# Kernel tuning notes

Measured on AMD Instinct MI355X. Metric: run time of the kernel, lower is better.

## Reference

```python
import jax, jax.numpy as jnp
import numpy as np

H_DIM = 64      # input_dim of edge_aggregation (== h_dim)
HID = 128       # hidden_size of each per-edge-type agg MLP
T = 5           # edge_types for non-nba dataset
B, E, N = 64, 1024, 512


def setup_inputs() -> dict:
    key = jax.random.key(0)
    ks = jax.random.split(key, 8)
    edge_distribution = jax.random.uniform(ks[0], (B, E, T), dtype=jnp.float32)
    H = jax.random.uniform(ks[1], (B, E, N), dtype=jnp.float32)
    ori = jax.random.normal(ks[2], (B, N, H_DIM), dtype=jnp.float32)
    s1 = 1.0 / np.sqrt(H_DIM)
    s2 = 1.0 / np.sqrt(HID)
    # stacked per-edge-type MLP params: Linear(64->128) -> ReLU -> Linear(128->64)
    W1 = jax.random.uniform(ks[3], (T, H_DIM, HID), minval=-s1, maxval=s1, dtype=jnp.float32)
    b1 = jax.random.uniform(ks[4], (T, HID), minval=-s1, maxval=s1, dtype=jnp.float32)
    W2 = jax.random.uniform(ks[5], (T, HID, H_DIM), minval=-s2, maxval=s2, dtype=jnp.float32)
    b2 = jax.random.uniform(ks[6], (T, H_DIM), minval=-s2, maxval=s2, dtype=jnp.float32)
    return {"edge_distribution": edge_distribution, "H": H, "ori": ori,
            "W1": W1, "b1": b1, "W2": W2, "b2": b2}


def reference(edge_distribution, H, ori, W1, b1, W2, b2):
    # incidence gather: hyperedge features [B, E, D]
    edges = jnp.matmul(H, ori)
    # per-edge-type 2-layer MLP, vectorized over the T edge types
    h = jax.nn.relu(jnp.einsum('bed,tdh->bteh', edges, W1) + b1[None, :, None, :])
    per_type = jnp.einsum('bteh,thd->bted', h, W2) + b2[None, :, None, :]
    # mixture-weighted sum over edge types -> [B, E, D]
    edge_feature = jnp.einsum('bet,bted->bed', edge_distribution, per_type)
    # scatter back through H^T and concat with original node features
    node_agg = jnp.einsum('ben,bed->bnd', H, edge_feature)  # H^T @ edge_feature
    node_feature = jnp.concatenate((node_agg, ori), axis=-1)  # [B, N, 2D]
    return node_feature
```

## Files before the change

### kernel.cpp

```cpp
#include <hip/hip_runtime.h>

#define B_   64
#define E_   1024
#define N_   512
#define D_   64
#define HID_ 128
#define T_   5

typedef __bf16 bf16x8 __attribute__((ext_vector_type(8)));
typedef float f32x4 __attribute__((ext_vector_type(4)));

__device__ __forceinline__ unsigned short f2bu(float f) {
    union { float f; unsigned int u; } v; v.f = f;
    unsigned int r = (v.u + 0x7fffu + ((v.u >> 16) & 1u)) >> 16;
    return (unsigned short)r;
}

__device__ __forceinline__ unsigned int pack2(float lo, float hi) {
    union { __bf16 b[2]; unsigned int u; } v;
    v.b[0] = (__bf16)lo; v.b[1] = (__bf16)hi;
    return v.u;
}

__device__ __forceinline__ uint4 cvt8(float4 a, float4 b) {
    union { __bf16 h[8]; uint4 u; } v;
    v.h[0] = (__bf16)a.x; v.h[1] = (__bf16)a.y; v.h[2] = (__bf16)a.z; v.h[3] = (__bf16)a.w;
    v.h[4] = (__bf16)b.x; v.h[5] = (__bf16)b.y; v.h[6] = (__bf16)b.z; v.h[7] = (__bf16)b.w;
    return v.u;
}

#define MFMA16(a, b, c) __builtin_amdgcn_mfma_f32_16x16x32_bf16((a), (b), (c), 0, 0, 0)

__global__ __launch_bounds__(256) void k_prep_w(const float* __restrict__ W1,
                                                const float* __restrict__ W2,
                                                unsigned short* __restrict__ W1T,
                                                unsigned short* __restrict__ W2T) {
    int idx = blockIdx.x * 256 + threadIdx.x;
    if (idx < T_ * HID_ * D_) {
        int t = idx / (HID_ * D_), rem = idx % (HID_ * D_);
        int h = rem / D_, d = rem % D_;
        W1T[idx] = f2bu(W1[(t * D_ + d) * HID_ + h]);
    } else {
        int j = idx - T_ * HID_ * D_;
        int t = j / (D_ * HID_), rem = j % (D_ * HID_);
        int d = rem / HID_, h = rem % HID_;
        W2T[j] = f2bu(W2[(t * HID_ + h) * D_ + d]);
    }
}

__global__ __launch_bounds__(256) void k_ori_prep(const float* __restrict__ ori,
                                                  float* __restrict__ out,
                                                  unsigned short* __restrict__ oriT) {
    int b = blockIdx.y, n0 = blockIdx.x * 64;
    __shared__ float tl[64 * 65];
    int tid = threadIdx.x;
    int dl = tid & 63;
    #pragma unroll 4
    for (int p = 0; p < 16; ++p) {
        int nn = p * 4 + (tid >> 6);
        float v = ori[(size_t)(b * N_ + n0 + nn) * D_ + dl];
        out[(size_t)(b * N_ + n0 + nn) * 128 + 64 + dl] = v;
        tl[dl * 65 + nn] = v;
    }
    __syncthreads();
    #pragma unroll 4
    for (int p = 0; p < 16; ++p) {
        int dd = p * 4 + (tid >> 6);
        oriT[(size_t)(b * D_ + dd) * N_ + n0 + dl] = f2bu(tl[dd * 65 + dl]);
    }
}

__global__ __launch_bounds__(256) void k_gemm_edges(const float* __restrict__ H,
                                                    const unsigned short* __restrict__ oriT,
                                                    unsigned short* __restrict__ edges) {
    int b = blockIdx.y, e0 = blockIdx.x * 128;
    __shared__ __align__(16) unsigned short aA[128 * 72];
    __shared__ __align__(16) unsigned short bB[64 * 72];
    int tid = threadIdx.x, w = tid >> 6, l = tid & 63, q = l >> 4, c = l & 15;
    const f32x4 zero = {0.f, 0.f, 0.f, 0.f};
    f32x4 acc[2][4];
    #pragma unroll
    for (int fm = 0; fm < 2; ++fm)
        #pragma unroll
        for (int fn = 0; fn < 4; ++fn) acc[fm][fn] = zero;

    for (int ks = 0; ks < 8; ++ks) {
        int k0 = ks * 64;
        #pragma unroll
        for (int p = 0; p < 4; ++p) {
            int u = p * 256 + tid, r = u >> 3, sg = u & 7;
            const float* s = &H[((size_t)b * E_ + e0 + r) * N_ + k0 + sg * 8];
            float4 f0 = *(const float4*)&s[0];
            float4 f1 = *(const float4*)&s[4];
            *(uint4*)&aA[r * 72 + sg * 8] = cvt8(f0, f1);
        }
        #pragma unroll
        for (int p = 0; p < 2; ++p) {
            int u = p * 256 + tid, r = u >> 3, sg = u & 7;
            *(uint4*)&bB[r * 72 + sg * 8] =
                *(const uint4*)&oriT[((size_t)b * D_ + r) * N_ + k0 + sg * 8];
        }
        __syncthreads();
        #pragma unroll
        for (int h = 0; h < 2; ++h) {
            bf16x8 a0 = *(const bf16x8*)&aA[(w * 32 + c) * 72 + h * 32 + q * 8];
            bf16x8 a1 = *(const bf16x8*)&aA[(w * 32 + 16 + c) * 72 + h * 32 + q * 8];
            #pragma unroll
            for (int fn = 0; fn < 4; ++fn) {
                bf16x8 bb = *(const bf16x8*)&bB[(fn * 16 + c) * 72 + h * 32 + q * 8];
                acc[0][fn] = MFMA16(a0, bb, acc[0][fn]);
                acc[1][fn] = MFMA16(a1, bb, acc[1][fn]);
            }
        }
        __syncthreads();
    }
    #pragma unroll
    for (int fm = 0; fm < 2; ++fm)
        #pragma unroll
        for (int fn = 0; fn < 4; ++fn)
            #pragma unroll
            for (int i = 0; i < 4; ++i) {
                int e = e0 + w * 32 + fm * 16 + q * 4 + i;
                int d = fn * 16 + c;
                edges[((size_t)b * E_ + e) * D_ + d] = f2bu(acc[fm][fn][i]);
            }
}

__global__ __launch_bounds__(256) void k_mlp(const unsigned short* __restrict__ edges,
                                             const float* __restrict__ ed,
                                             const float* __restrict__ b1,
                                             const float* __restrict__ b2,
                                             const unsigned short* __restrict__ W1T,
                                             const unsigned short* __restrict__ W2T,
                                             unsigned short* __restrict__ efT) {
    int bx = blockIdx.x;
    int b = bx >> 4, e0 = (bx & 15) * 64;
    __shared__ __align__(16) unsigned short a_sh[64 * 72];
    __shared__ __align__(16) unsigned short w_sh[128 * 72];
    __shared__ __align__(16) unsigned short h_sh[64 * 136];
    __shared__ float wd_sh[320];
    __shared__ float b1_sh[640];
    __shared__ float b2_sh[320];
    int tid = threadIdx.x, w = tid >> 6, l = tid & 63, q = l >> 4, c = l & 15;

    #pragma unroll
    for (int p = 0; p < 2; ++p) {
        int u = p * 256 + tid, r = u >> 3, sg = u & 7;
        *(uint4*)&a_sh[r * 72 + sg * 8] =
            *(const uint4*)&edges[((size_t)b * E_ + e0 + r) * D_ + sg * 8];
    }
    for (int u = tid; u < 320; u += 256) wd_sh[u] = ed[((size_t)b * E_ + e0) * T_ + u];
    for (int u = tid; u < 640; u += 256) b1_sh[u] = b1[u];
    for (int u = tid; u < 320; u += 256) b2_sh[u] = b2[u];

    const f32x4 zero = {0.f, 0.f, 0.f, 0.f};
    f32x4 y[4];
    #pragma unroll
    for (int fn = 0; fn < 4; ++fn) y[fn] = zero;

    for (int t = 0; t < T_; ++t) {
        __syncthreads();
        #pragma unroll
        for (int p = 0; p < 4; ++p) {
            int u = p * 256 + tid, hh = u >> 3, sg = u & 7;
            *(uint4*)&w_sh[hh * 72 + sg * 8] =
                *(const uint4*)&W1T[(t * HID_ + hh) * D_ + sg * 8];
        }
        __syncthreads();
        f32x4 hc[8];
        #pragma unroll
        for (int fn = 0; fn < 8; ++fn) hc[fn] = zero;
        #pragma unroll
        for (int ks = 0; ks < 2; ++ks) {
            bf16x8 a = *(const bf16x8*)&a_sh[(w * 16 + c) * 72 + ks * 32 + q * 8];
            #pragma unroll
            for (int fn = 0; fn < 8; ++fn) {
                bf16x8 bb = *(const bf16x8*)&w_sh[(fn * 16 + c) * 72 + ks * 32 + q * 8];
                hc[fn] = MFMA16(a, bb, hc[fn]);
            }
        }
        float wv[4];
        #pragma unroll
        for (int i = 0; i < 4; ++i) wv[i] = wd_sh[(w * 16 + q * 4 + i) * T_ + t];
        #pragma unroll
        for (int fn = 0; fn < 8; ++fn) {
            float b1v = b1_sh[t * HID_ + fn * 16 + c];
            #pragma unroll
            for (int i = 0; i < 4; ++i) {
                float v = hc[fn][i] + b1v;
                v = fmaxf(v, 0.0f) * wv[i];
                h_sh[(w * 16 + q * 4 + i) * 136 + fn * 16 + c] = f2bu(v);
            }
        }
        __syncthreads();
        #pragma unroll
        for (int p = 0; p < 4; ++p) {
            int u = p * 256 + tid, dd = u >> 4, sg = u & 15;
            *(uint4*)&w_sh[dd * 136 + sg * 8] =
                *(const uint4*)&W2T[(t * D_ + dd) * HID_ + sg * 8];
        }
        __syncthreads();
        #pragma unroll
        for (int ks = 0; ks < 4; ++ks) {
            bf16x8 a = *(const bf16x8*)&h_sh[(w * 16 + c) * 136 + ks * 32 + q * 8];
            #pragma unroll
            for (int fn = 0; fn < 4; ++fn) {
                bf16x8 bb = *(const bf16x8*)&w_sh[(fn * 16 + c) * 136 + ks * 32 + q * 8];
                y[fn] = MFMA16(a, bb, y[fn]);
            }
        }
    }
    #pragma unroll
    for (int fn = 0; fn < 4; ++fn) {
        int d = fn * 16 + c;
        ushort4 o;
        #pragma unroll
        for (int i = 0; i < 4; ++i) {
            int r = w * 16 + q * 4 + i;
            float s = y[fn][i];
            #pragma unroll
            for (int t = 0; t < T_; ++t) s += wd_sh[r * T_ + t] * b2_sh[t * D_ + d];
            ((unsigned short*)&o)[i] = f2bu(s);
        }
        *(ushort4*)&efT[((size_t)b * D_ + d) * E_ + e0 + w * 16 + q * 4] = o;
    }
}

__global__ __launch_bounds__(256) void k_gemm_out(const float* __restrict__ H,
                                                  const unsigned short* __restrict__ efT,
                                                  float* __restrict__ out) {
    int b = blockIdx.y, n0 = blockIdx.x * 64;
    __shared__ __align__(16) unsigned short aA[64 * 72];
    __shared__ unsigned int bB32[64 * 33];
    int tid = threadIdx.x, w = tid >> 6, l = tid & 63, q = l >> 4, c = l & 15;
    int r2 = tid >> 3, cg = tid & 7;
    const f32x4 zero = {0.f, 0.f, 0.f, 0.f};
    f32x4 acc[4];
    #pragma unroll
    for (int fm = 0; fm < 4; ++fm) acc[fm] = zero;

    for (int ks = 0; ks < 16; ++ks) {
        int k0 = ks * 64;
        #pragma unroll
        for (int p = 0; p < 2; ++p) {
            int u = p * 256 + tid, r = u >> 3, sg = u & 7;
            *(uint4*)&aA[r * 72 + sg * 8] =
                *(const uint4*)&efT[((size_t)b * D_ + r) * E_ + k0 + sg * 8];
        }
        {
            const float* s0 = &H[((size_t)b * E_ + k0 + 2 * r2) * N_ + n0 + cg * 8];
            const float* s1 = s0 + N_;
            float4 f0 = *(const float4*)&s0[0], f1 = *(const float4*)&s0[4];
            float4 g0 = *(const float4*)&s1[0], g1 = *(const float4*)&s1[4];
            float r0[8] = {f0.x, f0.y, f0.z, f0.w, f1.x, f1.y, f1.z, f1.w};
            float r1[8] = {g0.x, g0.y, g0.z, g0.w, g1.x, g1.y, g1.z, g1.w};
            #pragma unroll
            for (int j = 0; j < 8; ++j)
                bB32[(cg * 8 + j) * 33 + r2] = pack2(r0[j], r1[j]);
        }
        __syncthreads();
        #pragma unroll
        for (int h = 0; h < 2; ++h) {
            union { unsigned int u[4]; bf16x8 v; } bb;
            #pragma unroll
            for (int i = 0; i < 4; ++i)
                bb.u[i] = bB32[(w * 16 + c) * 33 + h * 16 + q * 4 + i];
            #pragma unroll
            for (int fm = 0; fm < 4; ++fm) {
                bf16x8 afr = *(const bf16x8*)&aA[(fm * 16 + c) * 72 + h * 32 + q * 8];
                acc[fm] = MFMA16(afr, bb.v, acc[fm]);
            }
        }
        __syncthreads();
    }
    #pragma unroll
    for (int fm = 0; fm < 4; ++fm) {
        *(f32x4*)&out[((size_t)b * N_ + n0 + w * 16 + c) * 128 + fm * 16 + q * 4] = acc[fm];
    }
}

extern "C" void kernel_launch(void* const* d_in, const int* in_sizes, int n_in,
                              void* d_out, int out_size, void* d_ws, size_t ws_size,
                              hipStream_t stream) {
    const float* ed  = (const float*)d_in[0];
    const float* H   = (const float*)d_in[1];
    const float* ori = (const float*)d_in[2];
    const float* W1  = (const float*)d_in[3];
    const float* b1  = (const float*)d_in[4];
    const float* W2  = (const float*)d_in[5];
    const float* b2  = (const float*)d_in[6];
    float* out = (float*)d_out;

    char* ws = (char*)d_ws;
    unsigned short* oriT  = (unsigned short*)ws; ws += (size_t)B_ * D_ * N_ * 2;
    unsigned short* W1T   = (unsigned short*)ws; ws += (size_t)T_ * HID_ * D_ * 2;
    unsigned short* W2T   = (unsigned short*)ws; ws += (size_t)T_ * D_ * HID_ * 2;
    unsigned short* edges = (unsigned short*)ws; ws += (size_t)B_ * E_ * D_ * 2;
    unsigned short* efT   = (unsigned short*)ws; ws += (size_t)B_ * D_ * E_ * 2;

    hipLaunchKernelGGL(k_prep_w, dim3(320), dim3(256), 0, stream, W1, W2, W1T, W2T);
    hipLaunchKernelGGL(k_ori_prep, dim3(8, 64), dim3(256), 0, stream, ori, out, oriT);
    hipLaunchKernelGGL(k_gemm_edges, dim3(8, 64), dim3(256), 0, stream, H, oriT, edges);
    hipLaunchKernelGGL(k_mlp, dim3(1024), dim3(256), 0, stream, edges, ed, b1, b2, W1T, W2T, efT);
    hipLaunchKernelGGL(k_gemm_out, dim3(8, 64), dim3(256), 0, stream, H, efT, out);
}
```

Baseline: 296.1 us.

## Fuse edge-feature GEMM into per-edge MLP kernel

The H@ori GEMM is merged into the MLP kernel, so each 64-edge block computes its edge features itself and writes them straight into shared memory. This drops the bf16 `edges` buffer in global memory along with its write and re-read, and removes one kernel launch. In exchange, each block uses a smaller 64-row GEMM tile and reloads the oriT slice twice as often. Shared memory per block also grows by two staging buffers, which may reduce occupancy.

```diff
diff --git a/kernel.cpp b/kernel.cpp
--- a/kernel.cpp
+++ b/kernel.cpp
@@ -70,71 +70,18 @@
     }
 }
 
-__global__ __launch_bounds__(256) void k_gemm_edges(const float* __restrict__ H,
-                                                    const unsigned short* __restrict__ oriT,
-                                                    unsigned short* __restrict__ edges) {
-    int b = blockIdx.y, e0 = blockIdx.x * 128;
-    __shared__ __align__(16) unsigned short aA[128 * 72];
-    __shared__ __align__(16) unsigned short bB[64 * 72];
-    int tid = threadIdx.x, w = tid >> 6, l = tid & 63, q = l >> 4, c = l & 15;
-    const f32x4 zero = {0.f, 0.f, 0.f, 0.f};
-    f32x4 acc[2][4];
-    #pragma unroll
-    for (int fm = 0; fm < 2; ++fm)
-        #pragma unroll
-        for (int fn = 0; fn < 4; ++fn) acc[fm][fn] = zero;
-
-    for (int ks = 0; ks < 8; ++ks) {
-        int k0 = ks * 64;
-        #pragma unroll
-        for (int p = 0; p < 4; ++p) {
-            int u = p * 256 + tid, r = u >> 3, sg = u & 7;
-            const float* s = &H[((size_t)b * E_ + e0 + r) * N_ + k0 + sg * 8];
-            float4 f0 = *(const float4*)&s[0];
-            float4 f1 = *(const float4*)&s[4];
-            *(uint4*)&aA[r * 72 + sg * 8] = cvt8(f0, f1);
-        }
-        #pragma unroll
-        for (int p = 0; p < 2; ++p) {
-            int u = p * 256 + tid, r = u >> 3, sg = u & 7;
-            *(uint4*)&bB[r * 72 + sg * 8] =
-                *(const uint4*)&oriT[((size_t)b * D_ + r) * N_ + k0 + sg * 8];
-        }
-        __syncthreads();
-        #pragma unroll
-        for (int h = 0; h < 2; ++h) {
-            bf16x8 a0 = *(const bf16x8*)&aA[(w * 32 + c) * 72 + h * 32 + q * 8];
-            bf16x8 a1 = *(const bf16x8*)&aA[(w * 32 + 16 + c) * 72 + h * 32 + q * 8];
-            #pragma unroll
-            for (int fn = 0; fn < 4; ++fn) {
-                bf16x8 bb = *(const bf16x8*)&bB[(fn * 16 + c) * 72 + h * 32 + q * 8];
-                acc[0][fn] = MFMA16(a0, bb, acc[0][fn]);
-                acc[1][fn] = MFMA16(a1, bb, acc[1][fn]);
-            }
-        }
-        __syncthreads();
-    }
-    #pragma unroll
-    for (int fm = 0; fm < 2; ++fm)
-        #pragma unroll
-        for (int fn = 0; fn < 4; ++fn)
-            #pragma unroll
-            for (int i = 0; i < 4; ++i) {
-                int e = e0 + w * 32 + fm * 16 + q * 4 + i;
-                int d = fn * 16 + c;
-                edges[((size_t)b * E_ + e) * D_ + d] = f2bu(acc[fm][fn][i]);
-            }
-}
-
-__global__ __launch_bounds__(256) void k_mlp(const unsigned short* __restrict__ edges,
-                                             const float* __restrict__ ed,
-                                             const float* __restrict__ b1,
-                                             const float* __restrict__ b2,
-                                             const unsigned short* __restrict__ W1T,
-                                             const unsigned short* __restrict__ W2T,
-                                             unsigned short* __restrict__ efT) {
+__global__ __launch_bounds__(256) void k_edge_mlp(const float* __restrict__ H,
+                                                  const unsigned short* __restrict__ oriT,
+                                                  const float* __restrict__ ed,
+                                                  const float* __restrict__ b1,
+                                                  const float* __restrict__ b2,
+                                                  const unsigned short* __restrict__ W1T,
+                                                  const unsigned short* __restrict__ W2T,
+                                                  unsigned short* __restrict__ efT) {
     int bx = blockIdx.x;
     int b = bx >> 4, e0 = (bx & 15) * 64;
+    __shared__ __align__(16) unsigned short aA[64 * 72];
+    __shared__ __align__(16) unsigned short bB[64 * 72];
     __shared__ __align__(16) unsigned short a_sh[64 * 72];
     __shared__ __align__(16) unsigned short w_sh[128 * 72];
     __shared__ __align__(16) unsigned short h_sh[64 * 136];
@@ -143,17 +90,50 @@
     __shared__ float b2_sh[320];
     int tid = threadIdx.x, w = tid >> 6, l = tid & 63, q = l >> 4, c = l & 15;
 
-    #pragma unroll
-    for (int p = 0; p < 2; ++p) {
-        int u = p * 256 + tid, r = u >> 3, sg = u & 7;
-        *(uint4*)&a_sh[r * 72 + sg * 8] =
-            *(const uint4*)&edges[((size_t)b * E_ + e0 + r) * D_ + sg * 8];
-    }
     for (int u = tid; u < 320; u += 256) wd_sh[u] = ed[((size_t)b * E_ + e0) * T_ + u];
     for (int u = tid; u < 640; u += 256) b1_sh[u] = b1[u];
     for (int u = tid; u < 320; u += 256) b2_sh[u] = b2[u];
 
     const f32x4 zero = {0.f, 0.f, 0.f, 0.f};
+
+    f32x4 acc1[4];
+    #pragma unroll
+    for (int fn = 0; fn < 4; ++fn) acc1[fn] = zero;
+
+    for (int ks = 0; ks < 8; ++ks) {
+        int k0 = ks * 64;
+        #pragma unroll
+        for (int p = 0; p < 2; ++p) {
+            int u = p * 256 + tid, r = u >> 3, sg = u & 7;
+            const float* s = &H[((size_t)b * E_ + e0 + r) * N_ + k0 + sg * 8];
+            float4 f0 = *(const float4*)&s[0];
+            float4 f1 = *(const float4*)&s[4];
+            *(uint4*)&aA[r * 72 + sg * 8] = cvt8(f0, f1);
+        }
+        #pragma unroll
+        for (int p = 0; p < 2; ++p) {
+            int u = p * 256 + tid, r = u >> 3, sg = u & 7;
+            *(uint4*)&bB[r * 72 + sg * 8] =
+                *(const uint4*)&oriT[((size_t)b * D_ + r) * N_ + k0 + sg * 8];
+        }
+        __syncthreads();
+        #pragma unroll
+        for (int h = 0; h < 2; ++h) {
+            bf16x8 a0 = *(const bf16x8*)&aA[(w * 16 + c) * 72 + h * 32 + q * 8];
+            #pragma unroll
+            for (int fn = 0; fn < 4; ++fn) {
+                bf16x8 bb = *(const bf16x8*)&bB[(fn * 16 + c) * 72 + h * 32 + q * 8];
+                acc1[fn] = MFMA16(a0, bb, acc1[fn]);
+            }
+        }
+        __syncthreads();
+    }
+    #pragma unroll
+    for (int fn = 0; fn < 4; ++fn)
+        #pragma unroll
+        for (int i = 0; i < 4; ++i)
+            a_sh[(w * 16 + q * 4 + i) * 72 + fn * 16 + c] = f2bu(acc1[fn][i]);
+
     f32x4 y[4];
     #pragma unroll
     for (int fn = 0; fn < 4; ++fn) y[fn] = zero;
@@ -292,15 +272,14 @@
     float* out = (float*)d_out;
 
     char* ws = (char*)d_ws;
-    unsigned short* oriT  = (unsigned short*)ws; ws += (size_t)B_ * D_ * N_ * 2;
-    unsigned short* W1T   = (unsigned short*)ws; ws += (size_t)T_ * HID_ * D_ * 2;
-    unsigned short* W2T   = (unsigned short*)ws; ws += (size_t)T_ * D_ * HID_ * 2;
-    unsigned short* edges = (unsigned short*)ws; ws += (size_t)B_ * E_ * D_ * 2;
-    unsigned short* efT   = (unsigned short*)ws; ws += (size_t)B_ * D_ * E_ * 2;
+    unsigned short* oriT = (unsigned short*)ws; ws += (size_t)B_ * D_ * N_ * 2;
+    unsigned short* W1T  = (unsigned short*)ws; ws += (size_t)T_ * HID_ * D_ * 2;
+    unsigned short* W2T  = (unsigned short*)ws; ws += (size_t)T_ * D_ * HID_ * 2;
+    unsigned short* efT  = (unsigned short*)ws; ws += (size_t)B_ * D_ * E_ * 2;
 
     hipLaunchKernelGGL(k_prep_w, dim3(320), dim3(256), 0, stream, W1, W2, W1T, W2T);
     hipLaunchKernelGGL(k_ori_prep, dim3(8, 64), dim3(256), 0, stream, ori, out, oriT);
-    hipLaunchKernelGGL(k_gemm_edges, dim3(8, 64), dim3(256), 0, stream, H, oriT, edges);
-    hipLaunchKernelGGL(k_mlp, dim3(1024), dim3(256), 0, stream, edges, ed, b1, b2, W1T, W2T, efT);
+    hipLaunchKernelGGL(k_edge_mlp, dim3(1024), dim3(256), 0, stream,
+                       H, oriT, ed, b1, b2, W1T, W2T, efT);
     hipLaunchKernelGGL(k_gemm_out, dim3(8, 64), dim3(256), 0, stream, H, efT, out);
 }
```

Result: faster. 276.8 us (-6.5%).
